# Kernel optimization log

Hardware: AMD Instinct MI355X
Metric: run time of the kernel (lower is better)

## Reference

```python
import jax, jax.numpy as jnp
import numpy as np


def _operators_3_to_2(x2d, A, norm):
    # x2d: [b, d, n, n], A: [b, n, n]. Returns the 20 basis tensors, each [b, d, n, n].
    t = lambda a: a.transpose(0, 1, 3, 2)
    shape = x2d.shape
    op1 = jnp.einsum('bdij,bij,bik->bdjk', x2d, A, A) / norm
    op2 = jnp.einsum('bdij,bij,bjk->bdik', x2d, A, A) / norm
    op3 = jnp.einsum('bdij,bik,bjk->bdij', x2d, A, A) / norm
    op4 = jnp.broadcast_to(jnp.einsum('bdij,bij->bdi', x2d, A)[..., None], shape) / norm
    op5 = jnp.broadcast_to(jnp.einsum('bdij,bij->bdj', x2d, A)[..., None], shape) / norm
    op6 = jnp.einsum('bdij,bik->bdjk', x2d, A) / norm
    # NOTE: source has ops7 = [op6, op6.transpose] (bug: op7 computed but unused) -- replicated faithfully.
    op8 = jnp.einsum('bdij,bik->bdij', x2d, A) / norm
    op9 = jnp.einsum('bdij,bjk->bdij', x2d, A) / norm
    op10 = jnp.broadcast_to(x2d.sum(3, keepdims=True), shape) / norm
    op11 = jnp.broadcast_to(x2d.sum(2, keepdims=True), shape) / norm
    return [op1, t(op1), op2, t(op2), op3,
            op4, t(op4), op5, t(op5),
            op6, t(op6), op6, t(op6),
            op8, op9,
            op10, t(op10), op11, t(op11),
            x2d]


def _forward(x, edge_weight, coeffs1, bias1, coeffs2, bias2, edge_index, batch, n):
    f = x.shape[-1]
    b = x.shape[0] // n
    # to_2d_tensor: [b*n, f] -> [b, 2f, n, n]
    x2 = x.reshape(b, n, f).transpose(0, 2, 1)  # [b, f, n]
    x_2d = jnp.concatenate([
        jnp.broadcast_to(x2[:, :, :, None], (b, f, n, n)),
        jnp.broadcast_to(x2[:, :, None, :], (b, f, n, n)),
    ], axis=1)
    # to_dense_adj: scatter-add edge weights into per-graph dense [b, n, n]
    g = batch[edge_index[0]]
    r = edge_index[0] - g * n
    c = edge_index[1] - g * n
    A = jnp.zeros((b, n, n), x.dtype).at[g, r, c].add(edge_weight)
    norm = jnp.asarray(n, x.dtype)  # normalization=True default
    for li, (coeffs, bias) in enumerate([(coeffs1, bias1), (coeffs2, bias2)]):
        ops_out = jnp.stack(_operators_3_to_2(x_2d, A, norm), axis=2)  # [b, d, 20, n, n]
        x_2d = jnp.einsum('der,bdrij->beij', coeffs, ops_out) + bias
        if li == 0:
            x_2d = jax.nn.sigmoid(x_2d)
    return x_2d.mean(axis=(1, 2, 3))  # [b]


def setup_inputs() -> dict:
    key = jax.random.key(0)
    kx, kg, ks, kd, kw, kc1, kc2 = jax.random.split(key, 7)
    b, n, deg, f, h = 4, 128, 16, 32, 32
    d_in, d_out = 2 * f, 2 * h  # layer doubles channels; hidden layer is d_out -> d_out
    E = b * n * deg
    x = jax.random.normal(kx, (b * n, f), dtype=jnp.float32)
    g = jax.random.randint(kg, (E,), 0, b)
    src = jax.random.randint(ks, (E,), 0, n)
    dst = jax.random.randint(kd, (E,), 0, n)
    edge_index = jnp.stack([g * n + src, g * n + dst]).astype(jnp.int32)
    edge_weight = jax.random.uniform(kw, (E,), dtype=jnp.float32)
    batch = (jnp.arange(b * n) // n).astype(jnp.int32)
    scale1 = np.sqrt(2.0) / (d_in + d_out)
    scale2 = np.sqrt(2.0) / (d_out + d_out)
    coeffs1 = jax.random.normal(kc1, (d_in, d_out, 20), dtype=jnp.float32) * scale1
    coeffs2 = jax.random.normal(kc2, (d_out, d_out, 20), dtype=jnp.float32) * scale2
    bias1 = jnp.zeros((1, d_out, 1, 1), dtype=jnp.float32)
    bias2 = jnp.zeros((1, d_out, 1, 1), dtype=jnp.float32)
    return {"x": x, "edge_weight": edge_weight, "coeffs1": coeffs1, "bias1": bias1,
            "coeffs2": coeffs2, "bias2": bias2, "edge_index": edge_index,
            "batch": batch, "n": n}


def reference(x, edge_weight, coeffs1, bias1, coeffs2, bias2, edge_index, batch, n):
    return _forward(x, edge_weight, coeffs1, bias1, coeffs2, bias2, edge_index, batch, n)
```

## Files before the change

### kernel.cpp

```cpp
#include <hip/hip_runtime.h>
#include <stdint.h>

typedef unsigned short u16;
using short8 = __attribute__((ext_vector_type(8))) short;
using f32x4  = __attribute__((ext_vector_type(4))) float;

#define NB 4
#define NN 128
#define NF 32
#define ND 64
#define NMAT (NB*ND*NN*NN)

#define OFF_A     0u
#define OFF_ACC   262144u
#define OFF_AAT   262400u
#define OFF_RA    524544u
#define OFF_W     526592u
#define OFF_RM    1116416u
#define OFF_CM    1247488u
#define OFF_RX    1378560u
#define OFF_CX    1509632u
#define OFF_BF    1640960u
#define OFF_ATB   1641472u
#define OFF_WB    1772544u
#define OFF_X2    1936384u
#define OFF_XT    10324992u
#define OFF_UA    18713600u
#define OFF_UB    27102208u
#define OFF_UC    35490816u
#define OFF_UD    43879424u
#define OFF_YACC  52268032u
#define OFF_XF    (OFF_YACC)
#define OFF_EWF   (OFF_YACC + 65536u)
#define OFF_CF    (OFF_YACC + 98304u)

__device__ __forceinline__ float b2f(u16 v){
  union { uint32_t u; float f; } x; x.u = ((uint32_t)v) << 16; return x.f;
}
__device__ __forceinline__ u16 f2b(float f){
  union { uint32_t u; float f2; } x; x.f2 = f;
  uint32_t u = x.u;
  return (u16)((u + 0x7FFFu + ((u >> 16) & 1u)) >> 16);
}

#define MFMA16(a,b,c) __builtin_amdgcn_mfma_f32_16x16x32_bf16((a),(b),(c),0,0,0)

__device__ __constant__ signed char dR1[18] = {0,9,1,10,2,3,4,13,14,19,5,7,15,18,6,8,16,17};
__device__ __constant__ signed char dR2[18] = {-1,11,-1,12,-1,-1,-1,-1,-1,-1,-1,-1,-1,-1,-1,-1,-1,-1};

__global__ void k_convert(const void* __restrict__ xs, const void* __restrict__ ews,
                          const void* __restrict__ c1s, const void* __restrict__ c2s,
                          const void* __restrict__ b1s, const void* __restrict__ b2s,
                          float* __restrict__ xf, float* __restrict__ ewf,
                          float* __restrict__ cf, float* __restrict__ bfv){
  __shared__ int flg;
  const u16* x16 = (const u16*)xs;
  if (threadIdx.x == 0) flg = 0;
  __syncthreads();
  int hit = 0;
  for (int k = threadIdx.x; k < 1024; k += 256){
    u16 u = x16[k];
    if (((u >> 7) & 0xFF) >= 0x90) hit = 1;
  }
  if (hit) flg = 1;
  __syncthreads();
  const int isf = flg;

  int t = blockIdx.x*256 + threadIdx.x;
  if (t >= 188544) return;
  const void* src; int idx; float* dst;
  if (t < 16384)      { src = xs;  idx = t;          dst = xf + idx; }
  else if (t < 24576) { src = ews; idx = t - 16384;  dst = ewf + idx; }
  else if (t < 106496){ src = c1s; idx = t - 24576;  dst = cf + idx; }
  else if (t < 188416){ src = c2s; idx = t - 106496; dst = cf + 81920 + idx; }
  else if (t < 188480){ src = b1s; idx = t - 188416; dst = bfv + idx; }
  else                { src = b2s; idx = t - 188480; dst = bfv + 64 + idx; }
  float v = isf ? ((const float*)src)[idx] : b2f(((const u16*)src)[idx]);
  *dst = v;
}

__global__ void k_setup(const int* __restrict__ ei, const int* __restrict__ bat,
                        const float* __restrict__ ewf, float* __restrict__ A, int E,
                        const float* __restrict__ xf, u16* __restrict__ Xt,
                        const float* __restrict__ cf, float* __restrict__ W,
                        u16* __restrict__ Wb){
  const int bx = blockIdx.x;
  if (bx < 32){
    for (int t = bx*256 + threadIdx.x; t < E; t += 32*256){
      int s = ei[t], dnode = ei[E + t];
      int g = bat[s];
      int r = s - g*NN, c = dnode - g*NN;
      atomicAdd(&A[(g*NN + r)*NN + c], ewf[t]);
    }
  } else if (bx < 32 + 2048){
    int gid = (bx - 32)*256 + threadIdx.x;
    if (gid >= NMAT/8) return;
    int d0 = (gid & 7)*8;
    int ij = (gid >> 3) & 16383;
    int b  = gid >> 17;
    int i = ij >> 7, j = ij & 127;
    const float* src = (d0 < NF) ? &xf[(b*NN + i)*NF + d0] : &xf[(b*NN + j)*NF + (d0 - NF)];
    float4 f0 = *(const float4*)src;
    float4 f1 = *(const float4*)(src + 4);
    short8 v;
    v[0]=(short)f2b(f0.x); v[1]=(short)f2b(f0.y); v[2]=(short)f2b(f0.z); v[3]=(short)f2b(f0.w);
    v[4]=(short)f2b(f1.x); v[5]=(short)f2b(f1.y); v[6]=(short)f2b(f1.z); v[7]=(short)f2b(f1.w);
    *(short8*)(Xt + ((size_t)(b*16384 + ij))*64 + d0) = v;
  } else {
    int gl = (bx - 2080)*256 + threadIdx.x;
    if (gl >= 2*1152*64) return;
    int L = gl / (1152*64);
    int rem = gl - L*1152*64;
    int row = rem >> 6, e = rem & 63;
    int slot = row >> 6, d = row & 63;
    const float* cc = cf + L*81920;
    int base = (d*64 + e)*20;
    float v = cc[base + dR1[slot]];
    if (dR2[slot] >= 0) v += cc[base + dR2[slot]];
    float scale = (slot == 9) ? 1.0f : (1.0f/128.0f);
    v *= scale;
    W[gl] = v;
    if (slot < 10)
      Wb[(((size_t)L*10 + slot)*64 + e)*64 + d] = f2b(v);
  }
}

__global__ __launch_bounds__(256) void k_prepA(const float* __restrict__ A, float* __restrict__ AAt,
                                               u16* __restrict__ ATb, float* __restrict__ rA){
  const int iq = blockIdx.x, b = blockIdx.y;
  const int t = threadIdx.x;
  if (iq < 8){
    int j = t & 127, ih = t >> 7;
    const float* Ab = A + b*NN*NN;
    float acc[8] = {0,0,0,0,0,0,0,0};
    for (int k = 0; k < NN; k++){
      float aj = Ab[j*NN + k];
      #pragma unroll
      for (int ii = 0; ii < 8; ii++){
        int i = iq*16 + ih*8 + ii;
        acc[ii] += Ab[i*NN + k] * aj;
      }
    }
    #pragma unroll
    for (int ii = 0; ii < 8; ii++){
      int i = iq*16 + ih*8 + ii;
      AAt[(b*NN + i)*NN + j] = acc[ii];
    }
  } else if (iq == 8){
    __shared__ float lds[128][129];
    for (int l = 0; l < 64; l++){
      int idx = l*256 + t;
      lds[idx >> 7][idx & 127] = A[b*16384 + idx];
    }
    __syncthreads();
    for (int l = 0; l < 64; l++){
      int idx = l*256 + t;
      int r = idx >> 7, c = idx & 127;
      ATb[b*16384 + idx] = f2b(lds[c][r]);
    }
  } else {
    if (t < 128){
      const float* Ab = A + (b*NN + t)*NN;
      float s = 0.f;
      for (int j = 0; j < 128; j++) s += Ab[j];
      rA[b*NN + t] = s;
    }
  }
}

__global__ __launch_bounds__(256) void k_xt(const u16* __restrict__ X, u16* __restrict__ Xt){
  int b = blockIdx.y;
  int ij0 = blockIdx.x*64;
  __shared__ u16 lds[64][65];
  int t = threadIdx.x;
  #pragma unroll
  for (int l = 0; l < 2; l++){
    int idx = l*2048 + t*8;
    int d = idx >> 6, c = idx & 63;
    const u16* p = X + ((size_t)(b*64 + d))*16384 + ij0 + c;
    short8 v = *(const short8*)p;
    #pragma unroll
    for (int k = 0; k < 8; k++) lds[d][c + k] = (u16)v[k];
  }
  __syncthreads();
  #pragma unroll
  for (int l = 0; l < 2; l++){
    int idx = l*2048 + t*8;
    int r = idx >> 6, c = idx & 63;
    short8 v;
    #pragma unroll
    for (int k = 0; k < 8; k++) v[k] = (short)lds[c + k][r];
    *(short8*)(Xt + ((size_t)(b*16384 + ij0 + r))*64 + c) = v;
  }
}

#define SJ32 70
#define SJF  67

__global__ __launch_bounds__(256) void k_mixrow(const u16* __restrict__ Xt, const float* __restrict__ A,
    const float* __restrict__ AAt, const float* __restrict__ rA, const u16* __restrict__ Wb,
    u16* __restrict__ Ua, u16* __restrict__ Ub, u16* __restrict__ Uc, u16* __restrict__ Ud,
    float* __restrict__ Yacc,
    float* __restrict__ RM, float* __restrict__ CM,
    float* __restrict__ RX, float* __restrict__ CXv)
{
  const int b = blockIdx.y;
  const int t = threadIdx.x;

  if (blockIdx.x >= 256){
    int d = t & 63;
    int task = (blockIdx.x - 256)*4 + (t >> 6);
    float sm = 0.f, sx = 0.f;
    if (task < 128){
      int i = task;
      for (int j = 0; j < 128; j++){
        float xv = b2f(Xt[((size_t)(b*16384 + i*128 + j))*64 + d]);
        float av = A[b*16384 + i*128 + j];
        sm += xv*av; sx += xv;
      }
      RM[(b*64 + d)*128 + i] = sm;
      RX[(b*64 + d)*128 + i] = sx;
    } else {
      int j = task - 128;
      for (int i = 0; i < 128; i++){
        float xv = b2f(Xt[((size_t)(b*16384 + i*128 + j))*64 + d]);
        float av = A[b*16384 + i*128 + j];
        sm += xv*av; sx += xv;
      }
      CM[(b*64 + d)*128 + j] = sm;
      CXv[(b*64 + d)*128 + j] = sx;
    }
    return;
  }

  const int w = t >> 6, lane = t & 63;
  const int col = lane & 15, quad = lane >> 4;
  const int ij0 = blockIdx.x*64;

  __shared__ uint32_t lsb[4][32*SJ32];
  __shared__ float lsf[64*SJF];

  short8 wa[10][2];
  #pragma unroll
  for (int s = 0; s < 10; s++){
    const u16* wp = Wb + (size_t)((s*64 + w*16 + col)*64 + quad*8);
    wa[s][0] = *(const short8*)wp;
    wa[s][1] = *(const short8*)(wp + 32);
  }
  short8 xb[4][2];
  #pragma unroll
  for (int sj = 0; sj < 4; sj++){
    const u16* xp = Xt + ((size_t)(b*16384 + ij0 + sj*16 + col))*64 + quad*8;
    xb[sj][0] = *(const short8*)xp;
    xb[sj][1] = *(const short8*)(xp + 32);
  }
  float a_s[4], t_s[4], rjv[4];
  #pragma unroll
  for (int sj = 0; sj < 4; sj++){
    int ij = ij0 + sj*16 + col;
    a_s[sj] = A[b*16384 + ij];
    t_s[sj] = AAt[b*16384 + ij];
    rjv[sj] = rA[b*128 + (ij & 127)];
  }
  const float riv = rA[b*128 + (ij0 >> 7)];

  #pragma unroll
  for (int g = 0; g < 5; g++){
    const int s0_tab[5]  = {0, 2, 4, 5, 6};
    const int nsl_tab[5] = {2, 2, 1, 1, 4};
    const int s0 = s0_tab[g], nsl = nsl_tab[g];
    #pragma unroll
    for (int sj = 0; sj < 4; sj++){
      f32x4 acc[4];
      #pragma unroll
      for (int s = 0; s < 4; s++) acc[s] = (f32x4){0.f,0.f,0.f,0.f};
      #pragma unroll
      for (int s = 0; s < 4; s++){
        if (s >= nsl) break;
        acc[s] = MFMA16(wa[s0+s][0], xb[sj][0], acc[s]);
        acc[s] = MFMA16(wa[s0+s][1], xb[sj][1], acc[s]);
      }
      if (g < 4){
        float v[4];
        #pragma unroll
        for (int r = 0; r < 4; r++){
          if (g == 2 || g == 3) v[r] = acc[0][r]*a_s[sj];
          else                  v[r] = acc[0][r]*a_s[sj] + acc[1][r];
        }
        uint32_t p0 = (uint32_t)f2b(v[0]) | ((uint32_t)f2b(v[1]) << 16);
        uint32_t p1 = (uint32_t)f2b(v[2]) | ((uint32_t)f2b(v[3]) << 16);
        int ep = w*8 + quad*2;
        lsb[g][ep*SJ32 + sj*16 + col] = p0;
        lsb[g][(ep + 1)*SJ32 + sj*16 + col] = p1;
      } else {
        #pragma unroll
        for (int r = 0; r < 4; r++){
          float v = acc[0][r]*t_s[sj] + acc[1][r]*riv + acc[2][r]*rjv[sj] + acc[3][r];
          lsf[(w*16 + quad*4 + r)*SJF + sj*16 + col] = v;
        }
      }
    }
  }
  __syncthreads();

  const int eo = t >> 2, seg = t & 3;
  const int ep = eo >> 1, sh = (eo & 1)*16;
  #pragma unroll
  for (int g = 0; g < 4; g++){
    const uint32_t* lp = &lsb[g][ep*SJ32 + seg*16];
    short8 v0, v1;
    #pragma unroll
    for (int k = 0; k < 8; k++){
      v0[k] = (short)((lp[k]   >> sh) & 0xffffu);
      v1[k] = (short)((lp[8+k] >> sh) & 0xffffu);
    }
    u16* U = (g==0)?Ua:(g==1)?Ub:(g==2)?Uc:Ud;
    u16* dst = U + ((size_t)(b*64 + eo) << 14) + ij0 + seg*16;
    *(short8*)dst = v0;
    *(short8*)(dst + 8) = v1;
  }
  {
    const float* fp = &lsf[eo*SJF + seg*16];
    float* dst = Yacc + ((size_t)(b*64 + eo) << 14) + ij0 + seg*16;
    #pragma unroll
    for (int q = 0; q < 4; q++)
      *(float4*)(dst + q*4) = make_float4(fp[q*4], fp[q*4+1], fp[q*4+2], fp[q*4+3]);
  }
}

#define SLT 68

__global__ __launch_bounds__(256) void k_tne(const u16* __restrict__ ATb,
    const u16* __restrict__ Ua, const u16* __restrict__ Ub,
    const u16* __restrict__ Uc, const u16* __restrict__ Ud,
    const float* __restrict__ Yacc, const float* __restrict__ W,
    const float* __restrict__ RM, const float* __restrict__ CM,
    const float* __restrict__ RX, const float* __restrict__ CXv,
    const float* __restrict__ bias, u16* __restrict__ Xout, float* __restrict__ acc4, int last)
{
  const int nh = blockIdx.x, be = blockIdx.y;
  const int b = be >> 6, e = be & 63;
  const int t = threadIdx.x, wave = t >> 6, lane = t & 63;
  const int col = lane & 15, quad = lane >> 4;
  const int m0 = (wave >> 1)*64;
  const int n0 = nh*64 + (wave & 1)*32;
  const int nb0 = nh*64;

  __shared__ uint32_t uls[128*SLT];
  __shared__ uint32_t ubl[64*SLT];
  __shared__ float radd[128], cadd[128];
  __shared__ float red[4];

  if (t < 128){
    int i = t; float s = 0.f;
    for (int d = 0; d < ND; d++){
      int v = (b*ND + d)*NN + i;
      s += W[(640 + d)*64 + e]*RM[v] + W[(704 + d)*64 + e]*CM[v]
         + W[(768 + d)*64 + e]*RX[v] + W[(832 + d)*64 + e]*CXv[v];
    }
    radd[i] = s;
  } else {
    int j = t - 128; float s = 0.f;
    for (int d = 0; d < ND; d++){
      int v = (b*ND + d)*NN + j;
      s += W[(896 + d)*64 + e]*RM[v] + W[(960 + d)*64 + e]*CM[v]
         + W[(1024 + d)*64 + e]*RX[v] + W[(1088 + d)*64 + e]*CXv[v];
    }
    cadd[j] = s;
  }

  const u16* ua = Ua + ((size_t)be << 14);
  const u16* ub = Ub + ((size_t)be << 14);
  {
    const int kp = t >> 2;
    #pragma unroll
    for (int it = 0; it < 4; it++){
      int mo = it*4 + (t & 3);
      short8 r0 = *(const short8*)(ua + (2*kp)*128 + mo*8);
      short8 r1 = *(const short8*)(ua + (2*kp + 1)*128 + mo*8);
      #pragma unroll
      for (int x = 0; x < 8; x++)
        uls[(mo*8 + x)*SLT + kp] = ((uint32_t)(u16)r0[x]) | (((uint32_t)(u16)r1[x]) << 16);
    }
    #pragma unroll
    for (int it = 0; it < 2; it++){
      int no = it*4 + (t & 3);
      short8 r0 = *(const short8*)(ub + (2*kp)*128 + nb0 + no*8);
      short8 r1 = *(const short8*)(ub + (2*kp + 1)*128 + nb0 + no*8);
      #pragma unroll
      for (int x = 0; x < 8; x++)
        ubl[(no*8 + x)*SLT + kp] = ((uint32_t)(u16)r0[x]) | (((uint32_t)(u16)r1[x]) << 16);
    }
  }
  __syncthreads();

  f32x4 acc[4][2];
  #pragma unroll
  for (int mt = 0; mt < 4; mt++)
    #pragma unroll
    for (int nt = 0; nt < 2; nt++)
      acc[mt][nt] = (f32x4){0.f,0.f,0.f,0.f};

  const u16* at = ATb + ((size_t)b << 14);
  short8 at_n[4][2];
  #pragma unroll
  for (int kq = 0; kq < 4; kq++){
    int k0 = kq*32 + quad*8;
    at_n[kq][0] = *(const short8*)(at + (n0 + col)*128 + k0);
    at_n[kq][1] = *(const short8*)(at + (n0 + 16 + col)*128 + k0);
  }

  #pragma unroll
  for (int kq = 0; kq < 4; kq++){
    int kd = kq*16 + quad*4;
    #pragma unroll
    for (int mt = 0; mt < 4; mt++){
      short8 af = *(const short8*)&uls[(m0 + mt*16 + col)*SLT + kd];
      acc[mt][0] = MFMA16(af, at_n[kq][0], acc[mt][0]);
      acc[mt][1] = MFMA16(af, at_n[kq][1], acc[mt][1]);
    }
  }
  #pragma unroll
  for (int kq = 0; kq < 4; kq++){
    int k0 = kq*32 + quad*8, kd = kq*16 + quad*4;
    short8 bf0 = *(const short8*)&ubl[((wave & 1)*32 + 0*16 + col)*SLT + kd];
    short8 bf1 = *(const short8*)&ubl[((wave & 1)*32 + 1*16 + col)*SLT + kd];
    #pragma unroll
    for (int mt = 0; mt < 4; mt++){
      short8 af = *(const short8*)(at + (m0 + mt*16 + col)*128 + k0);
      acc[mt][0] = MFMA16(af, bf0, acc[mt][0]);
      acc[mt][1] = MFMA16(af, bf1, acc[mt][1]);
    }
  }
  {
    const u16* uc = Uc + ((size_t)be << 14);
    #pragma unroll
    for (int kq = 0; kq < 4; kq++){
      int k0 = kq*32 + quad*8;
      #pragma unroll
      for (int mt = 0; mt < 4; mt++){
        short8 af = *(const short8*)(uc + (m0 + mt*16 + col)*128 + k0);
        acc[mt][0] = MFMA16(af, at_n[kq][0], acc[mt][0]);
        acc[mt][1] = MFMA16(af, at_n[kq][1], acc[mt][1]);
      }
    }
  }
  {
    const u16* ud = Ud + ((size_t)be << 14);
    #pragma unroll
    for (int kq = 0; kq < 4; kq++){
      int k0 = kq*32 + quad*8;
      short8 bf0 = *(const short8*)(ud + (n0 + col)*128 + k0);
      short8 bf1 = *(const short8*)(ud + (n0 + 16 + col)*128 + k0);
      #pragma unroll
      for (int mt = 0; mt < 4; mt++){
        short8 af = *(const short8*)(at + (m0 + mt*16 + col)*128 + k0);
        acc[mt][0] = MFMA16(af, bf0, acc[mt][0]);
        acc[mt][1] = MFMA16(af, bf1, acc[mt][1]);
      }
    }
  }
  __syncthreads();

  uint32_t* stg = uls;
  const float bv = bias[e];
  const float* Y = Yacc + ((size_t)be << 14);
  if (!last){
    #pragma unroll
    for (int mt = 0; mt < 4; mt++)
      #pragma unroll
      for (int nt = 0; nt < 2; nt++)
        #pragma unroll
        for (int rp = 0; rp < 2; rp++){
          uint32_t p = 0;
          #pragma unroll
          for (int h = 0; h < 2; h++){
            int r = rp*2 + h;
            int row = m0 + mt*16 + quad*4 + r;
            int cn = n0 + nt*16 + col;
            float v = acc[mt][nt][r] + Y[row*128 + cn] + radd[row] + cadd[cn] + bv;
            v = 1.f/(1.f + __expf(-v));
            p |= ((uint32_t)f2b(v)) << (16*h);
          }
          int ipair = (m0 + mt*16 + quad*4) >> 1;
          stg[(ipair + rp)*SLT + (wave & 1)*32 + nt*16 + col] = p;
        }
    __syncthreads();
    const uint32_t* lp = &stg[(t >> 2)*SLT + (t & 1)*32];
    const int sh = ((t >> 1) & 1)*16;
    u16* dst = Xout + ((size_t)be << 14) + (size_t)(t >> 1)*128 + nh*64 + (t & 1)*32;
    #pragma unroll
    for (int q2 = 0; q2 < 4; q2++){
      short8 v;
      #pragma unroll
      for (int k = 0; k < 8; k++) v[k] = (short)((lp[q2*8 + k] >> sh) & 0xffffu);
      *(short8*)(dst + q2*8) = v;
    }
  } else {
    float loc = 0.f;
    #pragma unroll
    for (int mt = 0; mt < 4; mt++)
      #pragma unroll
      for (int nt = 0; nt < 2; nt++)
        #pragma unroll
        for (int r = 0; r < 4; r++){
          int row = m0 + mt*16 + quad*4 + r;
          int cn = n0 + nt*16 + col;
          loc += acc[mt][nt][r] + Y[row*128 + cn] + radd[row] + cadd[cn] + bv;
        }
    for (int off = 32; off > 0; off >>= 1) loc += __shfl_down(loc, off, 64);
    if (lane == 0) red[wave] = loc;
    __syncthreads();
    if (t == 0) atomicAdd(&acc4[b], red[0] + red[1] + red[2] + red[3]);
  }
}

__global__ void k_finish(const float* __restrict__ acc4, const u16* __restrict__ x16,
                         void* __restrict__ out){
  __shared__ int flg;
  int t = threadIdx.x;
  if (t == 0) flg = 0;
  __syncthreads();
  int hit = 0;
  for (int k = t; k < 512; k += 64){
    u16 u = x16[k];
    if (((u >> 7) & 0xFF) >= 0x90) hit = 1;
  }
  if (hit) flg = 1;
  __syncthreads();
  if (t < NB){
    float v = acc4[t] * (1.0f/1048576.0f);
    if (flg) ((float*)out)[t] = v;
    else     ((u16*)out)[t] = f2b(v);
  }
}

extern "C" void kernel_launch(void* const* d_in, const int* in_sizes, int n_in,
                              void* d_out, int out_size, void* d_ws, size_t ws_size,
                              hipStream_t stream)
{
  const void* x   = d_in[0];
  const void* ew  = d_in[1];
  const void* c1  = d_in[2];
  const void* b1  = d_in[3];
  const void* c2  = d_in[4];
  const void* b2  = d_in[5];
  const int* ei  = (const int*)d_in[6];
  const int* bat = (const int*)d_in[7];
  const int E = in_sizes[1];

  char* wsb = (char*)d_ws;
  float* A    = (float*)(wsb + OFF_A);
  float* acc4 = (float*)(wsb + OFF_ACC);
  float* AAt  = (float*)(wsb + OFF_AAT);
  float* rA   = (float*)(wsb + OFF_RA);
  float* W    = (float*)(wsb + OFF_W);
  float* RM   = (float*)(wsb + OFF_RM);
  float* CM   = (float*)(wsb + OFF_CM);
  float* RX   = (float*)(wsb + OFF_RX);
  float* CXv  = (float*)(wsb + OFF_CX);
  float* bfv  = (float*)(wsb + OFF_BF);
  u16* ATb = (u16*)(wsb + OFF_ATB);
  u16* Wb  = (u16*)(wsb + OFF_WB);
  u16* X2  = (u16*)(wsb + OFF_X2);
  u16* Xt  = (u16*)(wsb + OFF_XT);
  u16* Ua  = (u16*)(wsb + OFF_UA);
  u16* Ub  = (u16*)(wsb + OFF_UB);
  u16* Uc  = (u16*)(wsb + OFF_UC);
  u16* Ud  = (u16*)(wsb + OFF_UD);
  float* Yacc = (float*)(wsb + OFF_YACC);
  float* xf   = (float*)(wsb + OFF_XF);
  float* ewf  = (float*)(wsb + OFF_EWF);
  float* cf   = (float*)(wsb + OFF_CF);

  hipMemsetAsync(wsb, 0, OFF_AAT, stream);

  k_convert<<<dim3(737), dim3(256), 0, stream>>>(x, ew, c1, c2, b1, b2, xf, ewf, cf, bfv);
  k_setup<<<dim3(2656), dim3(256), 0, stream>>>(ei, bat, ewf, A, E, xf, Xt, cf, W, Wb);
  k_prepA<<<dim3(10, NB), dim3(256), 0, stream>>>(A, AAt, ATb, rA);

  for (int L = 0; L < 2; L++){
    const float* Wl = W + (size_t)L*1152*64;
    const u16*  Wbl = Wb + (size_t)L*10*64*64;
    if (L == 1)
      k_xt<<<dim3(256, NB), dim3(256), 0, stream>>>(X2, Xt);
    k_mixrow<<<dim3(320, NB), dim3(256), 0, stream>>>(Xt, A, AAt, rA, Wbl,
                                                      Ua, Ub, Uc, Ud, Yacc, RM, CM, RX, CXv);
    k_tne<<<dim3(2, 256), dim3(256), 0, stream>>>(ATb, Ua, Ub, Uc, Ud, Yacc, Wl,
                                                  RM, CM, RX, CXv, bfv + L*64, X2, acc4, L);
  }
  k_finish<<<dim3(1), dim3(64), 0, stream>>>(acc4, (const u16*)x, d_out);
}
```

Baseline: 234.5 us.

## Use d-major X layout directly, drop transpose and convert kernels

Switches the X activation buffer from ij-major ([b][ij][d]) to d-major ([b][d][ij]) so layer 1 can read X2 directly, removing the k_xt transpose kernel. k_mixrow now transposes its tile through LDS to build MFMA operands, and its row/column reduction path is restructured per-d with vectorized loads. The k_convert kernel is folded into k_setup, which reads raw inputs with on-the-fly dtype handling. This saves two launches and a full-tensor transpose, at the cost of extra LDS traffic and syncs in k_mixrow.

```diff
diff --git a/kernel.cpp b/kernel.cpp
--- a/kernel.cpp
+++ b/kernel.cpp
@@ -24,15 +24,12 @@
 #define OFF_ATB   1641472u
 #define OFF_WB    1772544u
 #define OFF_X2    1936384u
-#define OFF_XT    10324992u
+#define OFF_XE    10324992u
 #define OFF_UA    18713600u
 #define OFF_UB    27102208u
 #define OFF_UC    35490816u
 #define OFF_UD    43879424u
 #define OFF_YACC  52268032u
-#define OFF_XF    (OFF_YACC)
-#define OFF_EWF   (OFF_YACC + 65536u)
-#define OFF_CF    (OFF_YACC + 98304u)
 
 __device__ __forceinline__ float b2f(u16 v){
   union { uint32_t u; float f; } x; x.u = ((uint32_t)v) << 16; return x.f;
@@ -48,11 +45,14 @@
 __device__ __constant__ signed char dR1[18] = {0,9,1,10,2,3,4,13,14,19,5,7,15,18,6,8,16,17};
 __device__ __constant__ signed char dR2[18] = {-1,11,-1,12,-1,-1,-1,-1,-1,-1,-1,-1,-1,-1,-1,-1,-1,-1};
 
-__global__ void k_convert(const void* __restrict__ xs, const void* __restrict__ ews,
-                          const void* __restrict__ c1s, const void* __restrict__ c2s,
-                          const void* __restrict__ b1s, const void* __restrict__ b2s,
-                          float* __restrict__ xf, float* __restrict__ ewf,
-                          float* __restrict__ cf, float* __restrict__ bfv){
+__global__ void k_setup(const int* __restrict__ ei, const int* __restrict__ bat,
+                        const void* __restrict__ ews, float* __restrict__ A, int E,
+                        const void* __restrict__ xs, u16* __restrict__ Xe,
+                        const void* __restrict__ c1s, const void* __restrict__ c2s,
+                        const void* __restrict__ b1s, const void* __restrict__ b2s,
+                        float* __restrict__ W, u16* __restrict__ Wb,
+                        float* __restrict__ bfv)
+{
   __shared__ int flg;
   const u16* x16 = (const u16*)xs;
   if (threadIdx.x == 0) flg = 0;
@@ -66,46 +66,43 @@
   __syncthreads();
   const int isf = flg;
 
-  int t = blockIdx.x*256 + threadIdx.x;
-  if (t >= 188544) return;
-  const void* src; int idx; float* dst;
-  if (t < 16384)      { src = xs;  idx = t;          dst = xf + idx; }
-  else if (t < 24576) { src = ews; idx = t - 16384;  dst = ewf + idx; }
-  else if (t < 106496){ src = c1s; idx = t - 24576;  dst = cf + idx; }
-  else if (t < 188416){ src = c2s; idx = t - 106496; dst = cf + 81920 + idx; }
-  else if (t < 188480){ src = b1s; idx = t - 188416; dst = bfv + idx; }
-  else                { src = b2s; idx = t - 188480; dst = bfv + 64 + idx; }
-  float v = isf ? ((const float*)src)[idx] : b2f(((const u16*)src)[idx]);
-  *dst = v;
-}
-
-__global__ void k_setup(const int* __restrict__ ei, const int* __restrict__ bat,
-                        const float* __restrict__ ewf, float* __restrict__ A, int E,
-                        const float* __restrict__ xf, u16* __restrict__ Xt,
-                        const float* __restrict__ cf, float* __restrict__ W,
-                        u16* __restrict__ Wb){
   const int bx = blockIdx.x;
   if (bx < 32){
+    if (bx == 0 && threadIdx.x < 128){
+      int tt = threadIdx.x;
+      const void* bsrc = (tt < 64) ? b1s : b2s;
+      int idx = tt & 63;
+      bfv[tt] = isf ? ((const float*)bsrc)[idx] : b2f(((const u16*)bsrc)[idx]);
+    }
     for (int t = bx*256 + threadIdx.x; t < E; t += 32*256){
       int s = ei[t], dnode = ei[E + t];
       int g = bat[s];
       int r = s - g*NN, c = dnode - g*NN;
-      atomicAdd(&A[(g*NN + r)*NN + c], ewf[t]);
+      float wv = isf ? ((const float*)ews)[t] : b2f(((const u16*)ews)[t]);
+      atomicAdd(&A[(g*NN + r)*NN + c], wv);
     }
   } else if (bx < 32 + 2048){
     int gid = (bx - 32)*256 + threadIdx.x;
-    if (gid >= NMAT/8) return;
-    int d0 = (gid & 7)*8;
-    int ij = (gid >> 3) & 16383;
-    int b  = gid >> 17;
-    int i = ij >> 7, j = ij & 127;
-    const float* src = (d0 < NF) ? &xf[(b*NN + i)*NF + d0] : &xf[(b*NN + j)*NF + (d0 - NF)];
-    float4 f0 = *(const float4*)src;
-    float4 f1 = *(const float4*)(src + 4);
+    int ij8 = gid & 2047;
+    int d   = (gid >> 11) & 63;
+    int b   = gid >> 17;
+    int ij  = ij8*8;
+    int i = ij >> 7, j0 = ij & 127;
     short8 v;
-    v[0]=(short)f2b(f0.x); v[1]=(short)f2b(f0.y); v[2]=(short)f2b(f0.z); v[3]=(short)f2b(f0.w);
-    v[4]=(short)f2b(f1.x); v[5]=(short)f2b(f1.y); v[6]=(short)f2b(f1.z); v[7]=(short)f2b(f1.w);
-    *(short8*)(Xt + ((size_t)(b*16384 + ij))*64 + d0) = v;
+    if (d < NF){
+      int idx = (b*NN + i)*NF + d;
+      u16 bv = isf ? f2b(((const float*)xs)[idx]) : ((const u16*)xs)[idx];
+      #pragma unroll
+      for (int k = 0; k < 8; k++) v[k] = (short)bv;
+    } else {
+      int dd = d - NF;
+      #pragma unroll
+      for (int k = 0; k < 8; k++){
+        int idx = (b*NN + j0 + k)*NF + dd;
+        v[k] = (short)(isf ? f2b(((const float*)xs)[idx]) : ((const u16*)xs)[idx]);
+      }
+    }
+    *(short8*)(Xe + ((size_t)(b*ND + d) << 14) + ij) = v;
   } else {
     int gl = (bx - 2080)*256 + threadIdx.x;
     if (gl >= 2*1152*64) return;
@@ -113,10 +110,14 @@
     int rem = gl - L*1152*64;
     int row = rem >> 6, e = rem & 63;
     int slot = row >> 6, d = row & 63;
-    const float* cc = cf + L*81920;
+    const void* cr = L ? c2s : c1s;
     int base = (d*64 + e)*20;
-    float v = cc[base + dR1[slot]];
-    if (dR2[slot] >= 0) v += cc[base + dR2[slot]];
+    int i1 = base + dR1[slot];
+    float v = isf ? ((const float*)cr)[i1] : b2f(((const u16*)cr)[i1]);
+    if (dR2[slot] >= 0){
+      int i2 = base + dR2[slot];
+      v += isf ? ((const float*)cr)[i2] : b2f(((const u16*)cr)[i2]);
+    }
     float scale = (slot == 9) ? 1.0f : (1.0f/128.0f);
     v *= scale;
     W[gl] = v;
@@ -168,36 +169,11 @@
   }
 }
 
-__global__ __launch_bounds__(256) void k_xt(const u16* __restrict__ X, u16* __restrict__ Xt){
-  int b = blockIdx.y;
-  int ij0 = blockIdx.x*64;
-  __shared__ u16 lds[64][65];
-  int t = threadIdx.x;
-  #pragma unroll
-  for (int l = 0; l < 2; l++){
-    int idx = l*2048 + t*8;
-    int d = idx >> 6, c = idx & 63;
-    const u16* p = X + ((size_t)(b*64 + d))*16384 + ij0 + c;
-    short8 v = *(const short8*)p;
-    #pragma unroll
-    for (int k = 0; k < 8; k++) lds[d][c + k] = (u16)v[k];
-  }
-  __syncthreads();
-  #pragma unroll
-  for (int l = 0; l < 2; l++){
-    int idx = l*2048 + t*8;
-    int r = idx >> 6, c = idx & 63;
-    short8 v;
-    #pragma unroll
-    for (int k = 0; k < 8; k++) v[k] = (short)lds[c + k][r];
-    *(short8*)(Xt + ((size_t)(b*16384 + ij0 + r))*64 + c) = v;
-  }
-}
-
 #define SJ32 70
 #define SJF  67
-
-__global__ __launch_bounds__(256) void k_mixrow(const u16* __restrict__ Xt, const float* __restrict__ A,
+#define SXE  34
+
+__global__ __launch_bounds__(256) void k_mixrow(const u16* __restrict__ Xe, const float* __restrict__ A,
     const float* __restrict__ AAt, const float* __restrict__ rA, const u16* __restrict__ Wb,
     u16* __restrict__ Ua, u16* __restrict__ Ub, u16* __restrict__ Uc, u16* __restrict__ Ud,
     float* __restrict__ Yacc,
@@ -208,24 +184,31 @@
   const int t = threadIdx.x;
 
   if (blockIdx.x >= 256){
-    int d = t & 63;
-    int task = (blockIdx.x - 256)*4 + (t >> 6);
+    const int d = blockIdx.x - 256;
+    const u16* Xd = Xe + ((size_t)(b*ND + d) << 14);
+    const float* Ab = A + b*NN*NN;
     float sm = 0.f, sx = 0.f;
-    if (task < 128){
-      int i = task;
-      for (int j = 0; j < 128; j++){
-        float xv = b2f(Xt[((size_t)(b*16384 + i*128 + j))*64 + d]);
-        float av = A[b*16384 + i*128 + j];
-        sm += xv*av; sx += xv;
+    if (t < 128){
+      const int i = t;
+      #pragma unroll 2
+      for (int j8 = 0; j8 < 16; j8++){
+        short8 xv = *(const short8*)(Xd + i*128 + j8*8);
+        float4 a0 = *(const float4*)(Ab + i*128 + j8*8);
+        float4 a1 = *(const float4*)(Ab + i*128 + j8*8 + 4);
+        float x0 = b2f((u16)xv[0]), x1 = b2f((u16)xv[1]), x2 = b2f((u16)xv[2]), x3 = b2f((u16)xv[3]);
+        float x4 = b2f((u16)xv[4]), x5 = b2f((u16)xv[5]), x6 = b2f((u16)xv[6]), x7 = b2f((u16)xv[7]);
+        sx += x0+x1+x2+x3+x4+x5+x6+x7;
+        sm += x0*a0.x + x1*a0.y + x2*a0.z + x3*a0.w
+            + x4*a1.x + x5*a1.y + x6*a1.z + x7*a1.w;
       }
       RM[(b*64 + d)*128 + i] = sm;
       RX[(b*64 + d)*128 + i] = sx;
     } else {
-      int j = task - 128;
+      const int j = t - 128;
       for (int i = 0; i < 128; i++){
-        float xv = b2f(Xt[((size_t)(b*16384 + i*128 + j))*64 + d]);
-        float av = A[b*16384 + i*128 + j];
-        sm += xv*av; sx += xv;
+        float xv = b2f(Xd[i*128 + j]);
+        sx += xv;
+        sm += xv * Ab[i*128 + j];
       }
       CM[(b*64 + d)*128 + j] = sm;
       CXv[(b*64 + d)*128 + j] = sx;
@@ -246,13 +229,6 @@
     const u16* wp = Wb + (size_t)((s*64 + w*16 + col)*64 + quad*8);
     wa[s][0] = *(const short8*)wp;
     wa[s][1] = *(const short8*)(wp + 32);
-  }
-  short8 xb[4][2];
-  #pragma unroll
-  for (int sj = 0; sj < 4; sj++){
-    const u16* xp = Xt + ((size_t)(b*16384 + ij0 + sj*16 + col))*64 + quad*8;
-    xb[sj][0] = *(const short8*)xp;
-    xb[sj][1] = *(const short8*)(xp + 32);
   }
   float a_s[4], t_s[4], rjv[4];
   #pragma unroll
@@ -263,6 +239,33 @@
     rjv[sj] = rA[b*128 + (ij & 127)];
   }
   const float riv = rA[b*128 + (ij0 >> 7)];
+
+  uint32_t* ldsX = &lsb[0][0];
+  {
+    const int ep = t >> 3;
+    const int s8 = (t & 7)*8;
+    const u16* xp = Xe + ((size_t)(b*ND + 2*ep) << 14) + ij0 + s8;
+    short8 r0 = *(const short8*)xp;
+    short8 r1 = *(const short8*)(xp + 16384);
+    #pragma unroll
+    for (int k = 0; k < 8; k++)
+      ldsX[(s8 + k)*SXE + ep] = ((uint32_t)(u16)r0[k]) | (((uint32_t)(u16)r1[k]) << 16);
+  }
+  __syncthreads();
+  short8 xb[4][2];
+  #pragma unroll
+  for (int sj = 0; sj < 4; sj++){
+    #pragma unroll
+    for (int h = 0; h < 2; h++){
+      const uint32_t* p = &ldsX[(sj*16 + col)*SXE + quad*4 + h*16];
+      uint2 u0 = *(const uint2*)p;
+      uint2 u1 = *(const uint2*)(p + 2);
+      union { uint32_t u[4]; short8 s; } cv;
+      cv.u[0] = u0.x; cv.u[1] = u0.y; cv.u[2] = u1.x; cv.u[3] = u1.y;
+      xb[sj][h] = cv.s;
+    }
+  }
+  __syncthreads();
 
   #pragma unroll
   for (int g = 0; g < 5; g++){
@@ -563,28 +566,24 @@
   u16* ATb = (u16*)(wsb + OFF_ATB);
   u16* Wb  = (u16*)(wsb + OFF_WB);
   u16* X2  = (u16*)(wsb + OFF_X2);
-  u16* Xt  = (u16*)(wsb + OFF_XT);
+  u16* Xe  = (u16*)(wsb + OFF_XE);
   u16* Ua  = (u16*)(wsb + OFF_UA);
   u16* Ub  = (u16*)(wsb + OFF_UB);
   u16* Uc  = (u16*)(wsb + OFF_UC);
   u16* Ud  = (u16*)(wsb + OFF_UD);
   float* Yacc = (float*)(wsb + OFF_YACC);
-  float* xf   = (float*)(wsb + OFF_XF);
-  float* ewf  = (float*)(wsb + OFF_EWF);
-  float* cf   = (float*)(wsb + OFF_CF);
 
   hipMemsetAsync(wsb, 0, OFF_AAT, stream);
 
-  k_convert<<<dim3(737), dim3(256), 0, stream>>>(x, ew, c1, c2, b1, b2, xf, ewf, cf, bfv);
-  k_setup<<<dim3(2656), dim3(256), 0, stream>>>(ei, bat, ewf, A, E, xf, Xt, cf, W, Wb);
+  k_setup<<<dim3(2656), dim3(256), 0, stream>>>(ei, bat, ew, A, E, x, Xe,
+                                                c1, c2, b1, b2, W, Wb, bfv);
   k_prepA<<<dim3(10, NB), dim3(256), 0, stream>>>(A, AAt, ATb, rA);
 
   for (int L = 0; L < 2; L++){
     const float* Wl = W + (size_t)L*1152*64;
     const u16*  Wbl = Wb + (size_t)L*10*64*64;
-    if (L == 1)
-      k_xt<<<dim3(256, NB), dim3(256), 0, stream>>>(X2, Xt);
-    k_mixrow<<<dim3(320, NB), dim3(256), 0, stream>>>(Xt, A, AAt, rA, Wbl,
+    const u16*  Xsrc = (L == 0) ? Xe : X2;
+    k_mixrow<<<dim3(320, NB), dim3(256), 0, stream>>>(Xsrc, A, AAt, rA, Wbl,
                                                       Ua, Ub, Uc, Ud, Yacc, RM, CM, RX, CXv);
     k_tne<<<dim3(2, 256), dim3(256), 0, stream>>>(ATb, Ua, Ub, Uc, Ud, Yacc, Wl,
                                                   RM, CM, RX, CXv, bfv + L*64, X2, acc4, L);
```

Result: faster. 223.0 us (-4.9%).
